# Optimization experiments

Hardware: AMD Instinct MI355X
Metric: run time of the kernel (lower is better)

Reference implementation:

```python
import jax, jax.numpy as jnp
import numpy as np

B, L, H, C = 2, 512, 128, 25

def setup_inputs() -> dict:
    key = jax.random.key(0)
    k1, k2, k3, k4 = jax.random.split(key, 4)
    x1 = jax.random.normal(k1, (B, L, H), dtype=jnp.float32)
    x2 = jax.random.normal(k2, (B, L, H), dtype=jnp.float32)
    W = jax.random.normal(k3, (C, 4 * H), dtype=jnp.float32) * (1.0 / np.sqrt(4 * H))
    b = jax.random.normal(k4, (C,), dtype=jnp.float32) * 0.01
    return {"x1": x1, "x2": x2, "W": W, "b": b}

def reference(x1, x2, W, b):
    # feat = cat([x1_i, x2_j, x1_i*x2_j, |x1_i - x2_j|]) over all (i, j) pairs,
    # then Linear(4H -> C). Split W into its 4 H-sized blocks so we never
    # materialize the [B, L, L, 4H] concatenated tensor.
    Hd = x1.shape[-1]
    W1, W2, W3, W4 = (W[:, 0:Hd], W[:, Hd:2*Hd], W[:, 2*Hd:3*Hd], W[:, 3*Hd:4*Hd])
    a = x1[:, :, None, :]   # [B, L, 1, H] -> row token
    c = x2[:, None, :, :]   # [B, 1, L, H] -> col token
    # a@W1 and c@W2 depend on only one index, so compute [B, L, C] then broadcast.
    t1 = jnp.einsum('blh,ch->blc', x1, W1)[:, :, None, :]  # [B, L, 1, C]
    t2 = jnp.einsum('blh,ch->blc', x2, W2)[:, None, :, :]  # [B, 1, L, C]
    # product term is a bilinear contraction; no [B,L,L,H] materialization needed.
    t3 = jnp.einsum('blh,bmh,ch->blmc', x1, x2, W3)         # [B, L, L, C]
    # abs-diff term requires the pairwise [B, L, L, H] tensor (nonlinear in pair).
    t4 = jnp.einsum('blmh,ch->blmc', jnp.abs(a - c), W4)    # [B, L, L, C]
    return t1 + t2 + t3 + t4 + b  # [B, L, L, C]
```

## Files before the change

kernel.cpp:

```cpp
#include <hip/hip_runtime.h>
#include <hip/hip_bf16.h>
#include <math.h>

#define BB 2
#define LL 512
#define HH 128
#define CC 25
#define W4H (4*HH)

typedef __attribute__((ext_vector_type(8))) short short8;
typedef __attribute__((ext_vector_type(4))) float f32x4;

#define T1_OFF 0
#define T2_OFF (BB*LL*CC)
#define WFT_BYTE_OFF (2*BB*LL*CC*4)

#define MTILE 64
#define LPB   8
#define XP    132

static __device__ __forceinline__ short f2bf(float f) {
    return __builtin_bit_cast(short, __float2bfloat16(f));
}

__global__ __launch_bounds__(256)
void prep_kernel(const float* __restrict__ x1, const float* __restrict__ x2,
                 const float* __restrict__ W, const float* __restrict__ bias,
                 float* __restrict__ ws)
{
    const int tid    = blockIdx.x * blockDim.x + threadIdx.x;
    const int stride = gridDim.x * blockDim.x;
    const int total  = BB * LL * CC;

    for (int idx = tid; idx < total; idx += stride) {
        const int c  = idx % CC;
        const int bl = idx / CC;
        const float* xr1 = x1 + (size_t)bl * HH;
        const float* xr2 = x2 + (size_t)bl * HH;
        const float* w1  = W + (size_t)c * W4H;
        const float* w2  = w1 + HH;
        float s1 = 0.f, s2 = 0.f;
        #pragma unroll 4
        for (int h = 0; h < HH; ++h) {
            s1 = fmaf(xr1[h], w1[h], s1);
            s2 = fmaf(xr2[h], w2[h], s2);
        }
        ws[T1_OFF + idx] = s1 + bias[c];
        ws[T2_OFF + idx] = s2;
    }

    unsigned short* wft = (unsigned short*)((char*)ws + WFT_BYTE_OFF);
    for (int idx = tid; idx < 32 * 256; idx += stride) {
        const int c = idx >> 8;
        const int k = idx & 255;
        float v = 0.f;
        if (c < CC) v = (k < HH) ? W[(size_t)c * W4H + 2*HH + k]
                                 : W[(size_t)c * W4H + 3*HH + (k - HH)];
        wft[idx] = (unsigned short)f2bf(v);
    }
}

__global__ __launch_bounds__(256)
void biaffine_mfma(const float* __restrict__ x1, const float* __restrict__ x2,
                   const float* __restrict__ ws, float* __restrict__ out)
{
    __shared__ __align__(16) float x2s[MTILE * XP];
    __shared__ __align__(16) float x1s[LPB * HH];

    const int tid = threadIdx.x;
    const int b   = blockIdx.z;
    const int l0  = blockIdx.y * LPB;
    const int m0  = blockIdx.x * MTILE;

    const int lane = tid & 63;
    const int wv   = tid >> 6;
    const int q    = lane >> 4;
    const int cn   = lane & 15;

    const unsigned short* wft = (const unsigned short*)((const char*)ws + WFT_BYTE_OFF);
    short8 Bf[2][8];
    #pragma unroll
    for (int t = 0; t < 2; ++t)
        #pragma unroll
        for (int kk = 0; kk < 8; ++kk)
            Bf[t][kk] = *(const short8*)(wft + ((cn + 16*t) * 256 + kk * 32 + q * 8));

    {
        const float* sx2 = x2 + ((size_t)b * LL + m0) * HH;
        #pragma unroll
        for (int i = 0; i < 8; ++i) {
            const int idx = i * 256 + tid;
            const int r   = idx >> 5;
            const int c4  = idx & 31;
            f32x4 v = *(const f32x4*)(sx2 + r * HH + c4 * 4);
            *(f32x4*)(&x2s[r * XP + c4 * 4]) = v;
        }
        const float* sx1 = x1 + ((size_t)b * LL + l0) * HH;
        f32x4 v = *(const f32x4*)(sx1 + tid * 4);
        *(f32x4*)(&x1s[tid * 4]) = v;
    }
    __syncthreads();

    const int mrowA = wv * 16 + cn;
    const float* px2 = &x2s[mrowA * XP];
    const float* Tb1 = ws + T1_OFF;
    const float* Tb2 = ws + T2_OFF;

    float t2a[4], t2b[4];
    #pragma unroll
    for (int r = 0; r < 4; ++r) {
        const int mg = m0 + wv * 16 + q * 4 + r;
        t2a[r] = Tb2[((size_t)b * LL + mg) * CC + cn];
        t2b[r] = (cn + 16 < CC) ? Tb2[((size_t)b * LL + mg) * CC + cn + 16] : 0.f;
    }

    for (int l = 0; l < LPB; ++l) {
        const float* px1 = &x1s[l * HH];
        f32x4 acc0 = {0.f, 0.f, 0.f, 0.f};
        f32x4 acc1 = {0.f, 0.f, 0.f, 0.f};

        #pragma unroll
        for (int hh = 0; hh < 4; ++hh) {
            const int hb = hh * 32 + q * 8;
            const f32x4 a0 = *(const f32x4*)(px1 + hb);
            const f32x4 a1 = *(const f32x4*)(px1 + hb + 4);
            const f32x4 b0 = *(const f32x4*)(px2 + hb);
            const f32x4 b1 = *(const f32x4*)(px2 + hb + 4);
            short8 Ap, Ad;
            #pragma unroll
            for (int j = 0; j < 4; ++j) {
                const float xa = a0[j], xb = b0[j];
                Ap[j] = f2bf(xa * xb);
                Ad[j] = f2bf(fabsf(xa - xb));
            }
            #pragma unroll
            for (int j = 0; j < 4; ++j) {
                const float xa = a1[j], xb = b1[j];
                Ap[4 + j] = f2bf(xa * xb);
                Ad[4 + j] = f2bf(fabsf(xa - xb));
            }
            acc0 = __builtin_amdgcn_mfma_f32_16x16x32_bf16(Ap, Bf[0][hh],     acc0, 0, 0, 0);
            acc1 = __builtin_amdgcn_mfma_f32_16x16x32_bf16(Ap, Bf[1][hh],     acc1, 0, 0, 0);
            acc0 = __builtin_amdgcn_mfma_f32_16x16x32_bf16(Ad, Bf[0][hh + 4], acc0, 0, 0, 0);
            acc1 = __builtin_amdgcn_mfma_f32_16x16x32_bf16(Ad, Bf[1][hh + 4], acc1, 0, 0, 0);
        }

        const int lg = l0 + l;
        const float t1a = Tb1[((size_t)b * LL + lg) * CC + cn];
        const float t1b = (cn + 16 < CC) ? Tb1[((size_t)b * LL + lg) * CC + cn + 16] : 0.f;
        #pragma unroll
        for (int r = 0; r < 4; ++r) {
            const int mg = m0 + wv * 16 + q * 4 + r;
            float* o = out + (((size_t)b * LL + lg) * LL + mg) * CC;
            o[cn] = acc0[r] + t1a + t2a[r];
            if (cn + 16 < CC) o[cn + 16] = acc1[r] + t1b + t2b[r];
        }
    }
}

extern "C" void kernel_launch(void* const* d_in, const int* in_sizes, int n_in,
                              void* d_out, int out_size, void* d_ws, size_t ws_size,
                              hipStream_t stream) {
    const float* x1   = (const float*)d_in[0];
    const float* x2   = (const float*)d_in[1];
    const float* W    = (const float*)d_in[2];
    const float* bias = (const float*)d_in[3];
    float* out = (float*)d_out;
    float* ws  = (float*)d_ws;

    prep_kernel<<<256, 256, 0, stream>>>(x1, x2, W, bias, ws);

    dim3 grid(LL / MTILE, LL / LPB, BB);
    biaffine_mfma<<<grid, 256, 0, stream>>>(x1, x2, ws, out);
}
```

Baseline: 107.8 us.

## Interchange l/h loops in biaffine MFMA kernel and vectorize prep GEMV

The main kernel now keeps accumulators for all LPB rows in registers and iterates hh outermost. Each x2 fragment is read from LDS once and reused across all rows, and more independent MFMAs are exposed for latency hiding. All output stores are deferred until the end. The prep kernel gets a 2D grid (rows × channel) with float4 vector loads and split accumulators instead of a strided scalar loop. The cost is higher register pressure from 16 f32x4 accumulators, which may reduce occupancy.

```diff
diff --git a/kernel.cpp b/kernel.cpp
--- a/kernel.cpp
+++ b/kernel.cpp
@@ -28,36 +28,48 @@
                  const float* __restrict__ W, const float* __restrict__ bias,
                  float* __restrict__ ws)
 {
-    const int tid    = blockIdx.x * blockDim.x + threadIdx.x;
-    const int stride = gridDim.x * blockDim.x;
-    const int total  = BB * LL * CC;
+    const int tid = threadIdx.x;
+    const int c   = blockIdx.y;
+    const int bl  = blockIdx.x * 256 + tid;
 
-    for (int idx = tid; idx < total; idx += stride) {
-        const int c  = idx % CC;
-        const int bl = idx / CC;
-        const float* xr1 = x1 + (size_t)bl * HH;
-        const float* xr2 = x2 + (size_t)bl * HH;
-        const float* w1  = W + (size_t)c * W4H;
-        const float* w2  = w1 + HH;
-        float s1 = 0.f, s2 = 0.f;
-        #pragma unroll 4
-        for (int h = 0; h < HH; ++h) {
-            s1 = fmaf(xr1[h], w1[h], s1);
-            s2 = fmaf(xr2[h], w2[h], s2);
+    if (blockIdx.y == 0) {
+        unsigned short* wft = (unsigned short*)((char*)ws + WFT_BYTE_OFF);
+        for (int idx = blockIdx.x * 256 + tid; idx < 32 * 256; idx += 4 * 256) {
+            const int cc = idx >> 8;
+            const int k  = idx & 255;
+            float v = 0.f;
+            if (cc < CC) v = (k < HH) ? W[(size_t)cc * W4H + 2*HH + k]
+                                      : W[(size_t)cc * W4H + 3*HH + (k - HH)];
+            wft[idx] = (unsigned short)f2bf(v);
         }
-        ws[T1_OFF + idx] = s1 + bias[c];
-        ws[T2_OFF + idx] = s2;
     }
 
-    unsigned short* wft = (unsigned short*)((char*)ws + WFT_BYTE_OFF);
-    for (int idx = tid; idx < 32 * 256; idx += stride) {
-        const int c = idx >> 8;
-        const int k = idx & 255;
-        float v = 0.f;
-        if (c < CC) v = (k < HH) ? W[(size_t)c * W4H + 2*HH + k]
-                                 : W[(size_t)c * W4H + 3*HH + (k - HH)];
-        wft[idx] = (unsigned short)f2bf(v);
+    const float* w1  = W + (size_t)c * W4H;
+    const float* w2  = w1 + HH;
+    const float* xr1 = x1 + (size_t)bl * HH;
+    const float* xr2 = x2 + (size_t)bl * HH;
+
+    float s1a = 0.f, s1b = 0.f, s2a = 0.f, s2b = 0.f;
+    #pragma unroll
+    for (int i = 0; i < 32; i += 2) {
+        const f32x4 a0 = *(const f32x4*)(xr1 + i*4);
+        const f32x4 a1 = *(const f32x4*)(xr1 + i*4 + 4);
+        const f32x4 b0 = *(const f32x4*)(xr2 + i*4);
+        const f32x4 b1 = *(const f32x4*)(xr2 + i*4 + 4);
+        const f32x4 u0 = *(const f32x4*)(w1 + i*4);
+        const f32x4 u1 = *(const f32x4*)(w1 + i*4 + 4);
+        const f32x4 v0 = *(const f32x4*)(w2 + i*4);
+        const f32x4 v1 = *(const f32x4*)(w2 + i*4 + 4);
+        #pragma unroll
+        for (int j = 0; j < 4; ++j) {
+            s1a = fmaf(a0[j], u0[j], s1a);
+            s1b = fmaf(a1[j], u1[j], s1b);
+            s2a = fmaf(b0[j], v0[j], s2a);
+            s2b = fmaf(b1[j], v1[j], s2b);
+        }
     }
+    ws[T1_OFF + bl * CC + c] = s1a + s1b + bias[c];
+    ws[T2_OFF + bl * CC + c] = s2a + s2b;
 }
 
 __global__ __launch_bounds__(256)
@@ -103,6 +115,39 @@
 
     const int mrowA = wv * 16 + cn;
     const float* px2 = &x2s[mrowA * XP];
+
+    f32x4 acc0[LPB], acc1[LPB];
+    #pragma unroll
+    for (int l = 0; l < LPB; ++l) {
+        acc0[l] = (f32x4){0.f, 0.f, 0.f, 0.f};
+        acc1[l] = (f32x4){0.f, 0.f, 0.f, 0.f};
+    }
+
+    #pragma unroll
+    for (int hh = 0; hh < 4; ++hh) {
+        const int hb = hh * 32 + q * 8;
+        const f32x4 b0 = *(const f32x4*)(px2 + hb);
+        const f32x4 b1 = *(const f32x4*)(px2 + hb + 4);
+        #pragma unroll
+        for (int l = 0; l < LPB; ++l) {
+            const float* px1 = &x1s[l * HH];
+            const f32x4 a0 = *(const f32x4*)(px1 + hb);
+            const f32x4 a1 = *(const f32x4*)(px1 + hb + 4);
+            short8 Ap, Ad;
+            #pragma unroll
+            for (int j = 0; j < 4; ++j) {
+                Ap[j]     = f2bf(a0[j] * b0[j]);
+                Ad[j]     = f2bf(fabsf(a0[j] - b0[j]));
+                Ap[4 + j] = f2bf(a1[j] * b1[j]);
+                Ad[4 + j] = f2bf(fabsf(a1[j] - b1[j]));
+            }
+            acc0[l] = __builtin_amdgcn_mfma_f32_16x16x32_bf16(Ap, Bf[0][hh],     acc0[l], 0, 0, 0);
+            acc1[l] = __builtin_amdgcn_mfma_f32_16x16x32_bf16(Ap, Bf[1][hh],     acc1[l], 0, 0, 0);
+            acc0[l] = __builtin_amdgcn_mfma_f32_16x16x32_bf16(Ad, Bf[0][hh + 4], acc0[l], 0, 0, 0);
+            acc1[l] = __builtin_amdgcn_mfma_f32_16x16x32_bf16(Ad, Bf[1][hh + 4], acc1[l], 0, 0, 0);
+        }
+    }
+
     const float* Tb1 = ws + T1_OFF;
     const float* Tb2 = ws + T2_OFF;
 
@@ -114,37 +159,8 @@
         t2b[r] = (cn + 16 < CC) ? Tb2[((size_t)b * LL + mg) * CC + cn + 16] : 0.f;
     }
 
+    #pragma unroll
     for (int l = 0; l < LPB; ++l) {
-        const float* px1 = &x1s[l * HH];
-        f32x4 acc0 = {0.f, 0.f, 0.f, 0.f};
-        f32x4 acc1 = {0.f, 0.f, 0.f, 0.f};
-
-        #pragma unroll
-        for (int hh = 0; hh < 4; ++hh) {
-            const int hb = hh * 32 + q * 8;
-            const f32x4 a0 = *(const f32x4*)(px1 + hb);
-            const f32x4 a1 = *(const f32x4*)(px1 + hb + 4);
-            const f32x4 b0 = *(const f32x4*)(px2 + hb);
-            const f32x4 b1 = *(const f32x4*)(px2 + hb + 4);
-            short8 Ap, Ad;
-            #pragma unroll
-            for (int j = 0; j < 4; ++j) {
-                const float xa = a0[j], xb = b0[j];
-                Ap[j] = f2bf(xa * xb);
-                Ad[j] = f2bf(fabsf(xa - xb));
-            }
-            #pragma unroll
-            for (int j = 0; j < 4; ++j) {
-                const float xa = a1[j], xb = b1[j];
-                Ap[4 + j] = f2bf(xa * xb);
-                Ad[4 + j] = f2bf(fabsf(xa - xb));
-            }
-            acc0 = __builtin_amdgcn_mfma_f32_16x16x32_bf16(Ap, Bf[0][hh],     acc0, 0, 0, 0);
-            acc1 = __builtin_amdgcn_mfma_f32_16x16x32_bf16(Ap, Bf[1][hh],     acc1, 0, 0, 0);
-            acc0 = __builtin_amdgcn_mfma_f32_16x16x32_bf16(Ad, Bf[0][hh + 4], acc0, 0, 0, 0);
-            acc1 = __builtin_amdgcn_mfma_f32_16x16x32_bf16(Ad, Bf[1][hh + 4], acc1, 0, 0, 0);
-        }
-
         const int lg = l0 + l;
         const float t1a = Tb1[((size_t)b * LL + lg) * CC + cn];
         const float t1b = (cn + 16 < CC) ? Tb1[((size_t)b * LL + lg) * CC + cn + 16] : 0.f;
@@ -152,8 +168,8 @@
         for (int r = 0; r < 4; ++r) {
             const int mg = m0 + wv * 16 + q * 4 + r;
             float* o = out + (((size_t)b * LL + lg) * LL + mg) * CC;
-            o[cn] = acc0[r] + t1a + t2a[r];
-            if (cn + 16 < CC) o[cn + 16] = acc1[r] + t1b + t2b[r];
+            o[cn] = acc0[l][r] + t1a + t2a[r];
+            if (cn + 16 < CC) o[cn + 16] = acc1[l][r] + t1b + t2b[r];
         }
     }
 }
@@ -168,7 +184,8 @@
     float* out = (float*)d_out;
     float* ws  = (float*)d_ws;
 
-    prep_kernel<<<256, 256, 0, stream>>>(x1, x2, W, bias, ws);
+    dim3 pgrid(BB * LL / 256, CC);
+    prep_kernel<<<pgrid, 256, 0, stream>>>(x1, x2, W, bias, ws);
 
     dim3 grid(LL / MTILE, LL / LPB, BB);
     biaffine_mfma<<<grid, 256, 0, stream>>>(x1, x2, ws, out);
```

Result: slower. 111.9 us (+3.9%).
